# Performance work log

Measured on AMD Instinct MI355X. Metric: run time of the kernel, lower is better.

The kernel has to match this reference:

```python
import jax, jax.numpy as jnp
import numpy as np
from jax import lax

# ---- static config (matches init_kwargs) ----
ORDER = 1
NPTS = ORDER + 1            # 2
JUNC_K = 300
LINE_K = 5000
NMS_SIZE = 3
JUNC_THRESH = 0.008
EPS = 1e-5
B, C, H, W = 4, 256, 160, 160
HID = C // 4                # 64
OUT_CH = [1, 1, 2, 1, 2, 4]  # lmap,jmap,joff,cmap,coff,lvec
NHEADS = len(OUT_CH)
MAXO = max(OUT_CH)          # pad conv2 out-channels to 4 per head
# channel-select indices from padded (NHEADS*MAXO) grouped-conv output
SEL = np.array([h * MAXO + c for h, k in enumerate(OUT_CH) for c in range(k)])
# lvec channel permutation from original forward (identity for order=1)
PERM = np.arange(OUT_CH[-1]).reshape(-1, 2, 2)
PERM[:, 1] = PERM[::-1, 1]
PERM = PERM.reshape(-1)


def setup_inputs() -> dict:
    key = jax.random.key(0)
    ks = jax.random.split(key, 9)
    features = jax.random.normal(ks[0], (B, C, H, W), jnp.float32)
    w1 = jax.random.normal(ks[1], (NHEADS * HID, C, 3, 3), jnp.float32) / np.sqrt(C * 9)
    b1 = 0.01 * jax.random.normal(ks[2], (NHEADS * HID,), jnp.float32)
    gamma = 1.0 + 0.1 * jax.random.normal(ks[3], (NHEADS * HID,), jnp.float32)
    beta = 0.01 * jax.random.normal(ks[4], (NHEADS * HID,), jnp.float32)
    mean = 0.1 * jax.random.normal(ks[5], (NHEADS * HID,), jnp.float32)
    var = jax.random.uniform(ks[6], (NHEADS * HID,), jnp.float32, 0.5, 1.5)
    w2 = jax.random.normal(ks[7], (NHEADS * MAXO, HID, 3, 3), jnp.float32) / np.sqrt(HID * 9)
    b2 = 0.01 * jax.random.normal(ks[8], (NHEADS * MAXO,), jnp.float32)
    return dict(features=features, w1=w1, b1=b1, gamma=gamma, beta=beta,
                mean=mean, var=var, w2=w2, b2=b2)


def _conv(x, w, b, groups=1):
    y = lax.conv_general_dilated(x, w, (1, 1), 'SAME',
                                 dimension_numbers=('NCHW', 'OIHW', 'NCHW'),
                                 feature_group_count=groups)
    return y + b[None, :, None, None]


def _nms(hm):  # hm: (1,H,W) -> suppress non-peaks
    mx = lax.reduce_window(hm, -jnp.inf, lax.max, (1, NMS_SIZE, NMS_SIZE),
                           (1, 1, 1), [(0, 0), (1, 1), (1, 1)])
    return jnp.where(hm == mx, hm, 0.0)


def _post(jm, joff, cm, coff, lv):
    """Per-sample postprocess. jm,cm:(1,H,W) joff,coff:(2,H,W) lv:(4,H,W).
    Returns (pts:(LINE_K,2,2) padded lines, mask:(LINE_K,) validity)."""
    # junctions: NMS + top-K + thresh mask + offset gather
    sj, ij = lax.top_k(_nms(jm).reshape(-1), JUNC_K)
    valid_j = sj >= JUNC_THRESH
    xy = jnp.stack([ij % W, ij // W], -1).astype(jm.dtype)
    junc = xy + joff.reshape(2, -1).T[ij] + 0.5
    junc = jnp.stack([jnp.clip(junc[:, 0], 0.0, W - 1e-4),
                      jnp.clip(junc[:, 1], 0.0, H - 1e-4)], -1)
    # lines: top-K centers + vector field gather (thresh=0 -> always full K)
    sc, ic = lax.top_k(cm.reshape(-1), LINE_K)
    cxy = jnp.stack([ic % W, ic // W], -1).astype(cm.dtype)
    center = cxy + coff.reshape(2, -1).T[ic] + 0.5
    lvr = lv.reshape(NPTS // 2 * 2, 2, -1).transpose(2, 0, 1)  # (HW,2,2)
    loi = center[:, None] + lvr[ic]                            # (L,2,2)
    loi = jnp.stack([jnp.clip(loi[..., 0], 0.0, W - 1e-4),
                     jnp.clip(loi[..., 1], 0.0, H - 1e-4)], -1)
    # pairwise squared-distance argmin of each endpoint to junctions
    d1 = ((loi[:, None, 0] - junc[None]) ** 2).sum(-1)
    d2 = ((loi[:, None, -1] - junc[None]) ** 2).sum(-1)
    big = jnp.asarray(1e18, d1.dtype)
    i1 = jnp.argmin(jnp.where(valid_j[None], d1, big), axis=-1)
    i2 = jnp.argmin(jnp.where(valid_j[None], d2, big), axis=-1)
    imin = jnp.minimum(i1, i2)
    imax = jnp.maximum(i1, i2)
    keep = imin != imax
    # unique (imin,imax) pairs via sorted-key dedup (matches torch.unique order)
    BIGK = JUNC_K * JUNC_K
    keyv = jnp.where(keep, imin * JUNC_K + imax, BIGK)
    sk = jnp.sort(keyv)
    first = jnp.concatenate([jnp.ones((1,), bool), sk[1:] != sk[:-1]]) & (sk < BIGK)
    a = jnp.where(first, sk // JUNC_K, 0)
    b = jnp.where(first, sk % JUNC_K, 0)
    pts = jnp.stack([junc[a], junc[b]], axis=1)  # (L,2,2)
    swap = pts[:, 0, 1] > pts[:, 1, 1]
    pts = jnp.where(swap[:, None, None], pts[:, ::-1], pts)
    return pts, first


def _maps(features, w1, b1, gamma, beta, mean, var, w2, b2):
    y = _conv(features, w1, b1)
    y = (y - mean[None, :, None, None]) * gamma[None, :, None, None] * \
        lax.rsqrt(var + EPS)[None, :, None, None] + beta[None, :, None, None]
    y = jax.nn.relu(y)
    y = _conv(y, w2, b2, groups=NHEADS)        # (B, NHEADS*MAXO, H, W)
    m = y[:, SEL]                              # (B, 11, H, W)
    lmap = jax.nn.sigmoid(m[:, 0:1])
    jmap = jax.nn.sigmoid(m[:, 1:2])
    joff = m[:, 2:4]
    cmap = jax.nn.sigmoid(m[:, 4:5])
    coff = m[:, 5:7]
    lvec = m[:, 7:][:, PERM]
    return lmap, jmap, joff, cmap, coff, lvec


def reference(features, w1, b1, gamma, beta, mean, var, w2, b2):
    lmap, jmap, joff, cmap, coff, lvec = _maps(features, w1, b1, gamma, beta,
                                               mean, var, w2, b2)
    loi, mask = jax.vmap(_post)(jmap, joff, cmap, coff, lvec)
    return lmap, jmap, joff, cmap, coff, lvec, loi, mask


if __name__ == '__main__':
    out = reference(**setup_inputs())
    for o in out:
        print(o.shape, o.dtype)
```

## Files before the change

### kernel.cpp

```cpp
#include <hip/hip_runtime.h>
#include <math.h>

#define IMG   160
#define HWSZ  25600
#define NB    4
#define CIN   256
#define COUT1 384
#define BIGK  90000

#define OFF_LMAP 0
#define OFF_JMAP 102400
#define OFF_JOFF 204800
#define OFF_CMAP 409600
#define OFF_COFF 512000
#define OFF_LVEC 716800
#define OFF_LOI  1126400
#define OFF_MASK 1206400

static const size_t WS_Y1    = 0;
static const size_t WS_JSORT = (size_t)NB * COUT1 * HWSZ * 4;
static const size_t WS_CSORT = WS_JSORT + (size_t)NB * 32768 * 8;
static const size_t WS_JUNC  = WS_CSORT + (size_t)NB * 32768 * 8;
static const size_t WS_JVAL  = WS_JUNC + (size_t)NB * 300 * 2 * 4;
static const size_t WS_LKEY  = WS_JVAL + (size_t)NB * 300 * 4;
static const size_t WS_WPK   = WS_LKEY + (size_t)NB * 8192 * 4;
static const size_t WS_AFTER_WPK = WS_WPK + (size_t)12 * 8 * 9 * 32 * 64 * 2;
static const size_t WS_BNS   = WS_AFTER_WPK;
static const size_t WS_JM    = WS_BNS + 384 * 4;
static const size_t WS_CM    = WS_JM + (size_t)NB * 300 * 8;
static const size_t WS_FPK   = WS_CM + (size_t)NB * 5000 * 8;
static const size_t WS_NEED_MIN = WS_FPK;
static const size_t WS_NEED_PK = WS_FPK + (size_t)NB * 8 * 162 * 162 * 128;

typedef unsigned long long u64;
typedef __attribute__((ext_vector_type(8))) short short8;
typedef __attribute__((ext_vector_type(4))) float f32x4;
typedef __attribute__((ext_vector_type(4))) int int4v;

union frag_u { short8 s8; u64 u[2]; int4v v; };

__device__ __forceinline__ float clip_coord(float v) {
    return fminf(fmaxf(v, 0.0f), 159.9999f);
}
__device__ __forceinline__ float sigmoidf(float v) {
    return 1.0f / (1.0f + expf(-v));
}
__device__ __forceinline__ unsigned short f2bf(float f) {
    unsigned u = __float_as_uint(f);
    return (unsigned short)((u + 0x7FFFu + ((u >> 16) & 1u)) >> 16);
}
__device__ __forceinline__ float bf2f(unsigned short h) {
    return __uint_as_float((unsigned)h << 16);
}

__device__ __forceinline__ void async_copy16(void* lds, const void* g) {
    __builtin_amdgcn_global_load_lds(
        (const __attribute__((address_space(1))) unsigned int*)g,
        (__attribute__((address_space(3))) unsigned int*)lds, 16, 0, 0);
}


__global__ void wpack_pk_kernel(const float* __restrict__ w1, short* __restrict__ wpk,
                                const float* __restrict__ gamma,
                                const float* __restrict__ var,
                                float* __restrict__ bns) {
    if (blockIdx.x == 6912) {
        for (int i = threadIdx.x; i < COUT1; i += 256)
            bns[i] = gamma[i] / sqrtf(var[i] + 1e-5f);
        return;
    }
    int e = blockIdx.x * 256 + threadIdx.x;
    int row = e >> 6, sp = e & 63;
    int ocl = row & 31;
    int tap = (row >> 5) % 9;
    int icc = (row / 288) & 7;
    int octile = row / 2304;
    int p16 = sp >> 3, j = sp & 7;
    int l16 = p16 ^ (ocl & 7);
    int ql = l16 * 8 + j;
    int term = ql >> 5, icl = ql & 31;
    int oc = octile * 32 + ocl, ic = icc * 32 + icl;
    float a = w1[((size_t)oc * CIN + ic) * 9 + tap];
    unsigned short hi = f2bf(a);
    wpk[e] = (term == 0) ? (short)hi : (short)f2bf(a - bf2f(hi));
}

__global__ __launch_bounds__(256) void pack_feat_kernel(
    const float* __restrict__ feat, short* __restrict__ fpk) {
    const int tid = threadIdx.x;
    const int c4  = (tid >> 4) & 3;
    const int r0  = (tid & 15) | (((tid >> 6) & 3) << 4);
    const int rest = blockIdx.x * 64 + r0;
    const int px = rest % 162;
    const int t2 = rest / 162;
    const int py = t2 % 162;
    const int bi = t2 / 162;
    const int s  = (2 * py + px) & 7;
    const int gy = py - 1, gx = px - 1;
    const bool valid = ((unsigned)gy < (unsigned)IMG) && ((unsigned)gx < (unsigned)IMG);
    const float* fs = feat + (size_t)(bi * 32 + c4 * 8) * HWSZ
                           + (valid ? gy * IMG + gx : 0);
    unsigned hi4[4], lo4[4];
#pragma unroll
    for (int j2 = 0; j2 < 4; ++j2) {
        float va = valid ? fs[(size_t)(2 * j2) * HWSZ]     : 0.0f;
        float vb = valid ? fs[(size_t)(2 * j2 + 1) * HWSZ] : 0.0f;
        unsigned short ha = f2bf(va), hb = f2bf(vb);
        unsigned short la = f2bf(va - bf2f(ha)), lb = f2bf(vb - bf2f(hb));
        hi4[j2] = (unsigned)ha | ((unsigned)hb << 16);
        lo4[j2] = (unsigned)la | ((unsigned)lb << 16);
    }
    const int p0 = c4 ^ s;
    const int p1 = (c4 | 4) ^ s;
    int4v* base = (int4v*)(fpk + (size_t)rest * 64);
    base[p0] = (int4v){ (int)hi4[0], (int)hi4[1], (int)hi4[2], (int)hi4[3] };
    base[p1] = (int4v){ (int)lo4[0], (int)lo4[1], (int)lo4[2], (int)lo4[3] };
}

__global__ __launch_bounds__(256, 2) void conv1_mfma_pk(
    const short* __restrict__ fpk, const short* __restrict__ wpk,
    const float* __restrict__ b1, const float* __restrict__ bns,
    const float* __restrict__ beta, const float* __restrict__ mean,
    float* __restrict__ y1) {
    const int bid   = blockIdx.x;
    const int slot  = bid >> 3;
    const int tile  = (bid & 7) + ((slot / 12) << 3);
    const int octile = slot - (slot / 12) * 12;
    const int bb = tile / 100, tt = tile % 100;
    const int ty = (tt / 10) * 16, tx = (tt % 10) * 16;
    const int oc0 = octile * 32;
    const int tid  = threadIdx.x;
    const int w    = tid >> 6;
    const int lane = tid & 63;
    const int quad = lane >> 4;
    const int l15  = lane & 15;
    const int wbase = tid & 192;

    __shared__ __align__(16) short Alds[288 * 64];
    __shared__ __align__(16) short Blds[324 * 64];

    int aoff[2];
#pragma unroll
    for (int t = 0; t < 2; ++t)
        aoff[t] = l15 * 128 + ((((t << 2) | quad) ^ (l15 & 7)) << 4);

    f32x4 acc[2][4];
#pragma unroll
    for (int mi = 0; mi < 2; ++mi)
#pragma unroll
        for (int nj = 0; nj < 4; ++nj) acc[mi][nj] = (f32x4){0.f, 0.f, 0.f, 0.f};

    const char* asrc0 = (const char*)wpk + (size_t)(octile * 8) * 36864;

    int boff[10];
#pragma unroll
    for (int it = 0; it < 10; ++it) {
        int k = it * 256 + tid;
        int hy = (int)((unsigned)k / 144u);
        int r  = k - hy * 144;
        boff[it] = hy * (162 * 128) + r * 16;
    }
    const int roff = 17 * (162 * 128) + (112 + (tid & 31)) * 16;
    const char* bsrc0 = (const char*)fpk
        + (((size_t)(bb * 8) * 162 + ty) * 162 + tx) * 128;
    const size_t bstride = (size_t)162 * 162 * 128;

    {
#pragma unroll
        for (int i = 0; i < 9; ++i)
            async_copy16((char*)Alds + (size_t)(i * 256 + wbase) * 16,
                         asrc0 + (size_t)(i * 256 + tid) * 16);
#pragma unroll
        for (int it = 0; it < 10; ++it)
            async_copy16((char*)Blds + (size_t)(it * 256 + wbase) * 16,
                         bsrc0 + boff[it]);
        if (tid < 32) {
            const int4v vv = *(const int4v*)(bsrc0 + roff);
            *(int4v*)((char*)Blds + (size_t)(2560 + tid) * 16) = vv;
        }
    }
    __syncthreads();

    int4v pvB[10]; int4v pvR;
#pragma unroll 1
    for (int icc = 0; icc < 8; ++icc) {
        if (icc < 7) {
            const char* bs = bsrc0 + (size_t)(icc + 1) * bstride;
#pragma unroll
            for (int it = 0; it < 10; ++it)
                pvB[it] = *(const int4v*)(bs + boff[it]);
            pvR = *(const int4v*)(bs + roff);
        }

#pragma unroll
        for (int sx = 0; sx < 3; ++sx) {
            frag_u Bf[2][6];
#pragma unroll
            for (int t = 0; t < 2; ++t)
#pragma unroll
                for (int rr = 0; rr < 6; ++rr) {
                    int pos = (w * 4 + rr) * 18 + (l15 + sx);
                    const char* bp = (const char*)Blds + (size_t)pos * 128
                        + ((((t << 2) | quad) ^ (pos & 7)) << 4);
                    Bf[t][rr].v = *(const int4v*)bp;
                }
#pragma unroll
            for (int sy = 0; sy < 3; ++sy) {
                const int tap = sy * 3 + sx;
                frag_u Af[2][2];
#pragma unroll
                for (int t = 0; t < 2; ++t)
#pragma unroll
                    for (int mi = 0; mi < 2; ++mi) {
                        const char* ap = (const char*)Alds
                            + (size_t)(tap * 32 + mi * 16) * 128 + aoff[t];
                        Af[t][mi].v = *(const int4v*)ap;
                    }
#pragma unroll
                for (int mi = 0; mi < 2; ++mi)
#pragma unroll
                    for (int nj = 0; nj < 4; ++nj) {
                        acc[mi][nj] = __builtin_amdgcn_mfma_f32_16x16x32_bf16(
                            Af[0][mi].s8, Bf[0][nj + sy].s8, acc[mi][nj], 0, 0, 0);
                        acc[mi][nj] = __builtin_amdgcn_mfma_f32_16x16x32_bf16(
                            Af[0][mi].s8, Bf[1][nj + sy].s8, acc[mi][nj], 0, 0, 0);
                        acc[mi][nj] = __builtin_amdgcn_mfma_f32_16x16x32_bf16(
                            Af[1][mi].s8, Bf[0][nj + sy].s8, acc[mi][nj], 0, 0, 0);
                    }
            }
        }

        if (icc < 7) {
            __syncthreads();
            {
                const char* as = asrc0 + (size_t)(icc + 1) * 36864;
#pragma unroll
                for (int i = 0; i < 9; ++i)
                    async_copy16((char*)Alds + (size_t)(i * 256 + wbase) * 16,
                                 as + (size_t)(i * 256 + tid) * 16);
            }
#pragma unroll
            for (int it = 0; it < 10; ++it)
                *(int4v*)((char*)Blds + (size_t)(it * 256 + tid) * 16) = pvB[it];
            if (tid < 32)
                *(int4v*)((char*)Blds + (size_t)(2560 + tid) * 16) = pvR;
            __syncthreads();
        }
    }

#pragma unroll
    for (int nj = 0; nj < 4; ++nj) {
        const int gy = ty + w * 4 + nj, gx = tx + l15;
#pragma unroll
        for (int mi = 0; mi < 2; ++mi)
#pragma unroll
            for (int r = 0; r < 4; ++r) {
                const int oc = oc0 + mi * 16 + quad * 4 + r;
                float v = acc[mi][nj][r] + b1[oc];
                v = (v - mean[oc]) * bns[oc] + beta[oc];
                y1[((size_t)(bb * COUT1 + oc)) * HWSZ + gy * IMG + gx] = fmaxf(v, 0.0f);
            }
    }
}


__global__ void wpack_kernel(const float* __restrict__ w1, short* __restrict__ wpk) {
    int e = blockIdx.x * 256 + threadIdx.x;
    int row = e >> 6, sp = e & 63;
    int ocl = row & 31;
    int tap = (row >> 5) % 9;
    int icc = (row / 288) & 7;
    int octile = row / 2304;
    int s = (sp >> 2) ^ (ocl & 15);
    int ql = s * 4 + (sp & 3);
    int term = ql >> 5, icl = ql & 31;
    int oc = octile * 32 + ocl, ic = icc * 32 + icl;
    float a = w1[((size_t)oc * CIN + ic) * 9 + tap];
    unsigned short hi = f2bf(a);
    wpk[e] = (term == 0) ? (short)hi : (short)f2bf(a - bf2f(hi));
}

__global__ __launch_bounds__(256, 2) void conv1_mfma(
    const float* __restrict__ feat, const short* __restrict__ wpk,
    const float* __restrict__ b1, const float* __restrict__ gamma,
    const float* __restrict__ beta, const float* __restrict__ mean,
    const float* __restrict__ var, float* __restrict__ y1) {
    const int bid   = blockIdx.x;
    const int slot  = bid >> 3;
    const int tile  = (bid & 7) + ((slot / 12) << 3);
    const int octile = slot - (slot / 12) * 12;
    const int bb = tile / 100, tt = tile % 100;
    const int ty = (tt / 10) * 16, tx = (tt % 10) * 16;
    const int oc0 = octile * 32;
    const int tid  = threadIdx.x;
    const int w    = tid >> 6;
    const int lane = tid & 63;
    const int quad = lane >> 4;
    const int l15  = lane & 15;

    __shared__ short Alds[288 * 64];
    __shared__ short Blds[324 * 68];

    int aoff[2][2];
#pragma unroll
    for (int t = 0; t < 2; ++t)
#pragma unroll
        for (int h = 0; h < 2; ++h)
            aoff[t][h] = l15 * 128 + (((t * 8 + quad * 2 + h) ^ l15) * 8);

    f32x4 acc[2][4];
#pragma unroll
    for (int mi = 0; mi < 2; ++mi)
#pragma unroll
        for (int nj = 0; nj < 4; ++nj) acc[mi][nj] = (f32x4){0.f, 0.f, 0.f, 0.f};

    const int4v* asrc_base = (const int4v*)wpk + (size_t)(octile * 8) * 2304;
    unsigned* Bd = (unsigned*)Blds;

    float pv0[21], pv1[21];

#pragma unroll
    for (int ii = 0; ii < 21; ++ii) {
        int i = tid + ii * 256;
        if (i < 5184) {
            int icp = i / 324, hp = i - icp * 324;
            int hy = hp / 18, hx = hp - hy * 18;
            int gy = ty + hy - 1, gx = tx + hx - 1;
            bool valid = ((unsigned)gy < IMG) && ((unsigned)gx < IMG);
            const float* fs = feat + ((size_t)(bb * CIN + icp * 2)) * HWSZ
                                   + (valid ? (gy * IMG + gx) : 0);
            pv0[ii] = valid ? fs[0]    : 0.0f;
            pv1[ii] = valid ? fs[HWSZ] : 0.0f;
        }
    }

#pragma unroll 1
    for (int icc = 0; icc < 8; ++icc) {
        __syncthreads();
        {
            const int4v* asrc = asrc_base + (size_t)icc * 2304;
            int4v* adst = (int4v*)Alds;
#pragma unroll
            for (int i = 0; i < 9; ++i)
                adst[tid + i * 256] = asrc[tid + i * 256];
        }
#pragma unroll
        for (int ii = 0; ii < 21; ++ii) {
            int i = tid + ii * 256;
            if (i < 5184) {
                int icp = i / 324, hp = i - icp * 324;
                float v0 = pv0[ii], v1 = pv1[ii];
                unsigned short h0 = f2bf(v0), h1 = f2bf(v1);
                unsigned short m0 = f2bf(v0 - bf2f(h0)), m1 = f2bf(v1 - bf2f(h1));
                Bd[hp * 34 + icp]      = (unsigned)h0 | ((unsigned)h1 << 16);
                Bd[hp * 34 + 16 + icp] = (unsigned)m0 | ((unsigned)m1 << 16);
            }
        }
        __syncthreads();

        if (icc < 7) {
#pragma unroll
            for (int ii = 0; ii < 21; ++ii) {
                int i = tid + ii * 256;
                if (i < 5184) {
                    int icp = i / 324, hp = i - icp * 324;
                    int hy = hp / 18, hx = hp - hy * 18;
                    int gy = ty + hy - 1, gx = tx + hx - 1;
                    bool valid = ((unsigned)gy < IMG) && ((unsigned)gx < IMG);
                    const float* fs = feat
                        + ((size_t)(bb * CIN + (icc + 1) * 32 + icp * 2)) * HWSZ
                        + (valid ? (gy * IMG + gx) : 0);
                    pv0[ii] = valid ? fs[0]    : 0.0f;
                    pv1[ii] = valid ? fs[HWSZ] : 0.0f;
                }
            }
        }

#pragma unroll
        for (int tap = 0; tap < 9; ++tap) {
            const int sy = tap / 3, sx = tap % 3;
            frag_u Af[2][2], Bf[2][4];
#pragma unroll
            for (int t = 0; t < 2; ++t) {
#pragma unroll
                for (int mi = 0; mi < 2; ++mi) {
                    const char* base = (const char*)Alds + (tap * 32 + mi * 16) * 128;
                    Af[t][mi].u[0] = *(const u64*)(base + aoff[t][0]);
                    Af[t][mi].u[1] = *(const u64*)(base + aoff[t][1]);
                }
#pragma unroll
                for (int nj = 0; nj < 4; ++nj) {
                    int pos = (w * 4 + nj + sy) * 18 + (l15 + sx);
                    const short* bp = &Blds[pos * 68 + t * 32 + quad * 8];
                    Bf[t][nj].u[0] = *(const u64*)bp;
                    Bf[t][nj].u[1] = *(const u64*)(bp + 4);
                }
            }
#pragma unroll
            for (int mi = 0; mi < 2; ++mi)
#pragma unroll
                for (int nj = 0; nj < 4; ++nj) {
                    acc[mi][nj] = __builtin_amdgcn_mfma_f32_16x16x32_bf16(
                        Af[0][mi].s8, Bf[0][nj].s8, acc[mi][nj], 0, 0, 0);
                    acc[mi][nj] = __builtin_amdgcn_mfma_f32_16x16x32_bf16(
                        Af[0][mi].s8, Bf[1][nj].s8, acc[mi][nj], 0, 0, 0);
                    acc[mi][nj] = __builtin_amdgcn_mfma_f32_16x16x32_bf16(
                        Af[1][mi].s8, Bf[0][nj].s8, acc[mi][nj], 0, 0, 0);
                    acc[mi][nj] = __builtin_amdgcn_mfma_f32_16x16x32_bf16(
                        Af[1][mi].s8, Bf[1][nj].s8, acc[mi][nj], 0, 0, 0);
                }
        }
    }

#pragma unroll
    for (int nj = 0; nj < 4; ++nj) {
        const int gy = ty + w * 4 + nj, gx = tx + l15;
#pragma unroll
        for (int mi = 0; mi < 2; ++mi)
#pragma unroll
            for (int r = 0; r < 4; ++r) {
                const int oc = oc0 + mi * 16 + quad * 4 + r;
                float v = acc[mi][nj][r] + b1[oc];
                v = (v - mean[oc]) * (gamma[oc] / sqrtf(var[oc] + 1e-5f)) + beta[oc];
                y1[((size_t)(bb * COUT1 + oc)) * HWSZ + gy * IMG + gx] = fmaxf(v, 0.0f);
            }
    }
}


__global__ __launch_bounds__(256, 2) void conv2_kernel(
    const float* __restrict__ y1, const float* __restrict__ w2,
    const float* __restrict__ b2, float* __restrict__ out) {
    const int KH[6]   = {1, 1, 2, 1, 2, 4};
    const int REG[6]  = {OFF_LMAP, OFF_JMAP, OFF_JOFF, OFF_CMAP, OFF_COFF, OFF_LVEC};
    const int SIGF[6] = {1, 1, 0, 1, 0, 0};

    const int bz = blockIdx.z;
    const int b  = bz / 6;
    const int h  = bz % 6;
    const int k  = KH[h];
    const int tx = blockIdx.x * 32, ty = blockIdx.y * 16;
    const int lx = threadIdx.x, ly = threadIdx.y;
    const int tid = ly * 16 + lx;

    __shared__ float tin[16][18][40];
    float* const tinf = &tin[0][0][0];
    float accv[4][2] = {{0.f,0.f},{0.f,0.f},{0.f,0.f},{0.f,0.f}};

    const float* yb = y1 + ((size_t)(b * COUT1 + h * 64)) * HWSZ;

    bool sok[3], sval[3];
    int  soff[3], sidx[3];
#pragma unroll
    for (int j = 0; j < 3; ++j) {
        int idx = tid + j * 256;
        sok[j] = (idx < 612);
        int r = idx / 34, col = idx - r * 34;
        int gy = ty - 1 + r, gx = tx - 1 + col;
        sval[j] = sok[j] && ((unsigned)gy < (unsigned)IMG) && ((unsigned)gx < (unsigned)IMG);
        soff[j] = sval[j] ? (gy * IMG + gx) : 0;
        sidx[j] = r * 40 + col;
    }

    for (int ic0 = 0; ic0 < 64; ic0 += 16) {
        __syncthreads();
#pragma unroll
        for (int j = 0; j < 3; ++j) {
            if (sok[j]) {
                const float* yp = yb + (size_t)ic0 * HWSZ + soff[j];
                float* tp = tinf + sidx[j];
#pragma unroll 4
                for (int c = 0; c < 16; ++c)
                    tp[c * 720] = sval[j] ? yp[(size_t)c * HWSZ] : 0.0f;
            }
        }
        __syncthreads();

        const float* tb = tinf + ly * 40 + 2 * lx;
#pragma unroll 2
        for (int c = 0; c < 16; ++c) {
            const float* tc = tb + c * 720;
            float n[3][4];
#pragma unroll
            for (int r = 0; r < 3; ++r) {
                float2 u = *(const float2*)(tc + r * 40);
                float2 v = *(const float2*)(tc + r * 40 + 2);
                n[r][0] = u.x; n[r][1] = u.y; n[r][2] = v.x; n[r][3] = v.y;
            }
#pragma unroll
            for (int o = 0; o < 4; ++o) {
                if (o < k) {
                    const float* wp = w2 + ((size_t)((h * 4 + o) * 64 + (ic0 + c))) * 9;
                    float a0 = accv[o][0], a1 = accv[o][1];
#pragma unroll
                    for (int r = 0; r < 3; ++r) {
                        float w0 = wp[3*r], w1 = wp[3*r+1], w2v = wp[3*r+2];
                        a0 = fmaf(n[r][0], w0, a0);
                        a1 = fmaf(n[r][1], w0, a1);
                        a0 = fmaf(n[r][1], w1, a0);
                        a1 = fmaf(n[r][2], w1, a1);
                        a0 = fmaf(n[r][2], w2v, a0);
                        a1 = fmaf(n[r][3], w2v, a1);
                    }
                    accv[o][0] = a0; accv[o][1] = a1;
                }
            }
        }
    }

    const int p = (ty + ly) * IMG + tx + 2 * lx;
#pragma unroll
    for (int o = 0; o < 4; ++o) {
        if (o < k) {
            float v0 = accv[o][0] + b2[h * 4 + o];
            float v1 = accv[o][1] + b2[h * 4 + o];
            if (SIGF[h]) { v0 = sigmoidf(v0); v1 = sigmoidf(v1); }
            size_t base = (size_t)REG[h] + ((size_t)(b * k + o)) * HWSZ + p;
            out[base]     = v0;
            out[base + 1] = v1;
        }
    }
}

__global__ void nms_pack_kernel(const float* __restrict__ out,
                                u64* __restrict__ jsort,
                                u64* __restrict__ csort) {
    const int g = blockIdx.x;
    const int b = g / 100, q = g % 100;
    const int p = q * 256 + threadIdx.x;
    const float* jm = out + OFF_JMAP + (size_t)b * HWSZ;
    const float* cm = out + OFF_CMAP + (size_t)b * HWSZ;

    const int x = p % IMG, y = p / IMG;
    float v = jm[p];
    float mx = v;
#pragma unroll
    for (int dy = -1; dy <= 1; ++dy)
#pragma unroll
        for (int dx = -1; dx <= 1; ++dx) {
            int nx = x + dx, ny = y + dy;
            if (nx >= 0 && nx < IMG && ny >= 0 && ny < IMG)
                mx = fmaxf(mx, jm[ny * IMG + nx]);
        }
    float nmsv = (v == mx) ? v : 0.0f;

    u64 tagj = ((u64)__float_as_uint(nmsv) << 32)
             | (u64)(0xFFFFFFFFu - (unsigned)p);
    u64 tagc = ((u64)__float_as_uint(cm[p]) << 32)
             | (u64)(0xFFFFFFFFu - (unsigned)p);
    jsort[(size_t)b * 32768 + p] = tagj;
    csort[(size_t)b * 32768 + p] = tagc;
    if (q < 28) {
        int pp = 25600 + q * 256 + threadIdx.x;
        jsort[(size_t)b * 32768 + pp] = 0ull;
        csort[(size_t)b * 32768 + pp] = 0ull;
    }
}

#define SK64(i) ((i) + ((i) >> 4))
__global__ __launch_bounds__(1024) void sort64_ldsA(u64* __restrict__ buf) {
    __shared__ u64 s[8192 + 512];
    const size_t base = (size_t)blockIdx.x * 8192;
    for (int i = threadIdx.x; i < 8192; i += 1024) s[SK64(i)] = buf[base + i];
    for (int k = 2; k <= 8192; k <<= 1)
        for (int j = k >> 1; j > 0; j >>= 1) {
            __syncthreads();
            for (int t = threadIdx.x; t < 4096; t += 1024) {
                int i = ((t & ~(j - 1)) << 1) | (t & (j - 1));
                int l = i | j;
                bool desc = ((i & k) == 0);
                u64 x = s[SK64(i)], y = s[SK64(l)];
                if (desc ? (x < y) : (x > y)) { s[SK64(i)] = y; s[SK64(l)] = x; }
            }
        }
    __syncthreads();
    for (int i = threadIdx.x; i < 8192; i += 1024) buf[base + i] = s[SK64(i)];
}

__device__ __forceinline__ int count_gt_desc(const u64* __restrict__ a, u64 e) {
    int cnt = 0;
#pragma unroll
    for (int st = 8192; st > 0; st >>= 1)
        if (cnt + st <= 8192 && a[cnt + st - 1] > e) cnt += st;
    return cnt;
}

__global__ void merge_topk_kernel(const u64* __restrict__ jsort,
                                  const u64* __restrict__ csort,
                                  u64* __restrict__ jm, u64* __restrict__ cm) {
    const int b = blockIdx.y;
    int t = blockIdx.x * 256 + threadIdx.x;
    const u64* src; u64* dst; int K, chunk, pos;
    if (t < 1200) {
        src = jsort + (size_t)b * 32768; dst = jm + (size_t)b * 300;
        K = 300; chunk = t / 300; pos = t - chunk * 300;
    } else {
        t -= 1200;
        if (t >= 20000) return;
        src = csort + (size_t)b * 32768; dst = cm + (size_t)b * 5000;
        K = 5000; chunk = t / 5000; pos = t - chunk * 5000;
    }
    u64 e = src[chunk * 8192 + pos];
    int rank = pos;
#pragma unroll
    for (int c = 0; c < 4; ++c)
        if (c != chunk) rank += count_gt_desc(src + c * 8192, e);
    if (rank < K) dst[rank] = e;
}

__global__ __launch_bounds__(1024) void sort32_lds(int* __restrict__ buf) {
    __shared__ int s[8192];
    int* a = buf + (size_t)blockIdx.x * 8192;
    for (int i = threadIdx.x; i < 8192; i += 1024) s[i] = a[i];
    for (int k = 2; k <= 8192; k <<= 1)
        for (int j = k >> 1; j > 0; j >>= 1) {
            __syncthreads();
            for (int t = threadIdx.x; t < 4096; t += 1024) {
                int i = ((t & ~(j - 1)) << 1) | (t & (j - 1));
                int l = i | j;
                bool asc = ((i & k) == 0);
                int x = s[i], y = s[l];
                if (asc ? (x > y) : (x < y)) { s[i] = y; s[l] = x; }
            }
        }
    __syncthreads();
    for (int i = threadIdx.x; i < 8192; i += 1024) a[i] = s[i];
}

__global__ void junction_kernel(const u64* __restrict__ jmk,
                                const float* __restrict__ out,
                                float* __restrict__ junc, int* __restrict__ jvalid) {
    const int b = blockIdx.x;
    const int t = threadIdx.x;
    if (t >= 300) return;
    u64 key = jmk[(size_t)b * 300 + t];
    float score  = __uint_as_float((unsigned)(key >> 32));
    unsigned idx = 0xFFFFFFFFu - (unsigned)(key & 0xFFFFFFFFull);
    const float* j0 = out + OFF_JOFF + (size_t)(b * 2) * HWSZ;
    const float* j1 = j0 + HWSZ;
    float jx = (float)(idx % IMG) + j0[idx] + 0.5f;
    float jy = (float)(idx / IMG) + j1[idx] + 0.5f;
    junc[(size_t)(b * 300 + t) * 2]     = clip_coord(jx);
    junc[(size_t)(b * 300 + t) * 2 + 1] = clip_coord(jy);
    jvalid[b * 300 + t] = (score >= 0.008f) ? 1 : 0;
}

__global__ void lines_kernel(const u64* __restrict__ cmk,
                             const float* __restrict__ junc,
                             const int* __restrict__ jvalid,
                             const float* __restrict__ out,
                             int* __restrict__ lkeys) {
    const int b = blockIdx.y;
    const int t = blockIdx.x * 256 + threadIdx.x;

    __shared__ float jx[300], jy[300];
    __shared__ int jv[300];
    for (int i = threadIdx.x; i < 300; i += 256) {
        jx[i] = junc[(size_t)(b * 300 + i) * 2];
        jy[i] = junc[(size_t)(b * 300 + i) * 2 + 1];
        jv[i] = jvalid[b * 300 + i];
    }
    __syncthreads();

    if (t >= 8192) return;
    if (t >= 5000) { lkeys[b * 8192 + t] = 0x7FFFFFFF; return; }

    u64 key = cmk[(size_t)b * 5000 + t];
    unsigned idx = 0xFFFFFFFFu - (unsigned)(key & 0xFFFFFFFFull);
    const float* c0 = out + OFF_COFF + (size_t)(b * 2) * HWSZ;
    const float* c1 = c0 + HWSZ;
    const float* lv = out + OFF_LVEC + (size_t)(b * 4) * HWSZ;

    float cx = (float)(idx % IMG) + c0[idx] + 0.5f;
    float cy = (float)(idx / IMG) + c1[idx] + 0.5f;
    float e0x = clip_coord(cx + lv[idx]);
    float e0y = clip_coord(cy + lv[HWSZ + idx]);
    float e1x = clip_coord(cx + lv[2 * HWSZ + idx]);
    float e1y = clip_coord(cy + lv[3 * HWSZ + idx]);

    float m1 = 1e18f, m2 = 1e18f;
    int i1 = 0, i2 = 0;
    for (int j = 0; j < 300; ++j) {
        if (jv[j]) {
            float dx = e0x - jx[j], dy = e0y - jy[j];
            float d = dx * dx + dy * dy;
            if (d < m1) { m1 = d; i1 = j; }
            dx = e1x - jx[j]; dy = e1y - jy[j];
            d = dx * dx + dy * dy;
            if (d < m2) { m2 = d; i2 = j; }
        }
    }
    int imin = min(i1, i2), imax = max(i1, i2);
    lkeys[b * 8192 + t] = (i1 != i2) ? (imin * 300 + imax) : BIGK;
}

__global__ void finalize_kernel(const int* __restrict__ lkeys,
                                const float* __restrict__ junc,
                                float* __restrict__ out) {
    const int b = blockIdx.y;
    const int t = blockIdx.x * 256 + threadIdx.x;
    if (t >= 5000) return;
    const int* lk = lkeys + b * 8192;
    int sk = lk[t];
    bool first = ((t == 0) || (sk != lk[t - 1])) && (sk < BIGK);
    int a  = first ? sk / 300 : 0;
    int bb = first ? sk % 300 : 0;
    float p0x = junc[(size_t)(b * 300 + a) * 2];
    float p0y = junc[(size_t)(b * 300 + a) * 2 + 1];
    float p1x = junc[(size_t)(b * 300 + bb) * 2];
    float p1y = junc[(size_t)(b * 300 + bb) * 2 + 1];
    if (p0y > p1y) {
        float tx = p0x; p0x = p1x; p1x = tx;
        float ty = p0y; p0y = p1y; p1y = ty;
    }
    size_t base = OFF_LOI + (size_t)(b * 5000 + t) * 4;
    out[base]     = p0x;
    out[base + 1] = p0y;
    out[base + 2] = p1x;
    out[base + 3] = p1y;
    out[OFF_MASK + b * 5000 + t] = first ? 1.0f : 0.0f;
}

extern "C" void kernel_launch(void* const* d_in, const int* in_sizes, int n_in,
                              void* d_out, int out_size, void* d_ws, size_t ws_size,
                              hipStream_t stream) {
    const float* feat  = (const float*)d_in[0];
    const float* w1    = (const float*)d_in[1];
    const float* b1    = (const float*)d_in[2];
    const float* gamma = (const float*)d_in[3];
    const float* beta  = (const float*)d_in[4];
    const float* mean  = (const float*)d_in[5];
    const float* var   = (const float*)d_in[6];
    const float* w2    = (const float*)d_in[7];
    const float* b2    = (const float*)d_in[8];
    float* out = (float*)d_out;
    char*  ws  = (char*)d_ws;

    if (ws_size < WS_NEED_MIN) return;

    float* y1 = (float*)(ws + WS_Y1);
    u64* jsort = (u64*)(ws + WS_JSORT);
    float* junc = (float*)(ws + WS_JUNC);
    int* jvalid = (int*)(ws + WS_JVAL);
    int* lkeys  = (int*)(ws + WS_LKEY);
    u64* csort = (u64*)(ws + WS_CSORT);
    short* wpk = (short*)(ws + WS_WPK);
    float* bns = (float*)(ws + WS_BNS);
    u64* jm    = (u64*)(ws + WS_JM);
    u64* cm    = (u64*)(ws + WS_CM);
    short* fpk = (short*)(ws + WS_FPK);

    if (ws_size >= WS_NEED_PK) {
        wpack_pk_kernel<<<dim3(6913), dim3(256), 0, stream>>>(w1, wpk, gamma, var, bns);
        pack_feat_kernel<<<dim3(13122), dim3(256), 0, stream>>>(feat, fpk);
        conv1_mfma_pk<<<dim3(4800), dim3(256), 0, stream>>>(
            fpk, wpk, b1, bns, beta, mean, y1);
    } else {
        wpack_kernel<<<dim3(6912), dim3(256), 0, stream>>>(w1, wpk);
        conv1_mfma<<<dim3(4800), dim3(256), 0, stream>>>(
            feat, wpk, b1, gamma, beta, mean, var, y1);
    }

    conv2_kernel<<<dim3(5, 10, NB * 6), dim3(16, 16), 0, stream>>>(y1, w2, b2, out);

    nms_pack_kernel<<<dim3(NB * 100), dim3(256), 0, stream>>>(out, jsort, csort);

    sort64_ldsA<<<dim3(32), dim3(1024), 0, stream>>>(jsort);

    merge_topk_kernel<<<dim3(83, NB), dim3(256), 0, stream>>>(jsort, csort, jm, cm);

    junction_kernel<<<dim3(NB), dim3(320), 0, stream>>>(jm, out, junc, jvalid);

    lines_kernel<<<dim3(32, NB), dim3(256), 0, stream>>>(cm, junc, jvalid, out, lkeys);

    sort32_lds<<<dim3(NB), dim3(1024), 0, stream>>>(lkeys);

    finalize_kernel<<<dim3(20, NB), dim3(256), 0, stream>>>(lkeys, junc, out);
}
```

Measured before the change: 950.4 us.

## Fuse prep, NMS+sort, and junction kernels; widen conv1 tiles with double-buffered weights

Merges weight packing, BN-scale and feature packing into one prep launch. It also folds the NMS key packing into the bitonic sort kernel, and removes the junction kernel by recomputing junction coordinates inside the lines and finalize kernels. conv1 now uses 512-thread blocks covering 16x32 output tiles, which shares the halo between two column halves. It double-buffers the weight tile in LDS so the next weight chunk streams in during compute. This cuts launch count and redundant global traffic, in exchange for higher LDS use per block and repeated coordinate recomputation in finalize.

Result: slower. 1.006 ms (+5.8%).

```diff
diff --git a/kernel.cpp b/kernel.cpp
--- a/kernel.cpp
+++ b/kernel.cpp
@@ -60,37 +60,38 @@
 }
 
 
-__global__ void wpack_pk_kernel(const float* __restrict__ w1, short* __restrict__ wpk,
-                                const float* __restrict__ gamma,
-                                const float* __restrict__ var,
-                                float* __restrict__ bns) {
-    if (blockIdx.x == 6912) {
-        for (int i = threadIdx.x; i < COUT1; i += 256)
+__global__ __launch_bounds__(256) void prep_kernel(
+    const float* __restrict__ w1, short* __restrict__ wpk,
+    const float* __restrict__ gamma, const float* __restrict__ var,
+    float* __restrict__ bns,
+    const float* __restrict__ feat, short* __restrict__ fpk) {
+    const int blk = blockIdx.x;
+    const int tid = threadIdx.x;
+    if (blk < 6912) {
+        int e = blk * 256 + tid;
+        int row = e >> 6, sp = e & 63;
+        int ocl = row & 31;
+        int tap = (row >> 5) % 9;
+        int icc = (row / 288) & 7;
+        int octile = row / 2304;
+        int p16 = sp >> 3, j = sp & 7;
+        int l16 = p16 ^ (ocl & 7);
+        int ql = l16 * 8 + j;
+        int term = ql >> 5, icl = ql & 31;
+        int oc = octile * 32 + ocl, ic = icc * 32 + icl;
+        float a = w1[((size_t)oc * CIN + ic) * 9 + tap];
+        unsigned short hi = f2bf(a);
+        wpk[e] = (term == 0) ? (short)hi : (short)f2bf(a - bf2f(hi));
+        return;
+    }
+    if (blk == 6912) {
+        for (int i = tid; i < COUT1; i += 256)
             bns[i] = gamma[i] / sqrtf(var[i] + 1e-5f);
         return;
     }
-    int e = blockIdx.x * 256 + threadIdx.x;
-    int row = e >> 6, sp = e & 63;
-    int ocl = row & 31;
-    int tap = (row >> 5) % 9;
-    int icc = (row / 288) & 7;
-    int octile = row / 2304;
-    int p16 = sp >> 3, j = sp & 7;
-    int l16 = p16 ^ (ocl & 7);
-    int ql = l16 * 8 + j;
-    int term = ql >> 5, icl = ql & 31;
-    int oc = octile * 32 + ocl, ic = icc * 32 + icl;
-    float a = w1[((size_t)oc * CIN + ic) * 9 + tap];
-    unsigned short hi = f2bf(a);
-    wpk[e] = (term == 0) ? (short)hi : (short)f2bf(a - bf2f(hi));
-}
-
-__global__ __launch_bounds__(256) void pack_feat_kernel(
-    const float* __restrict__ feat, short* __restrict__ fpk) {
-    const int tid = threadIdx.x;
     const int c4  = (tid >> 4) & 3;
     const int r0  = (tid & 15) | (((tid >> 6) & 3) << 4);
-    const int rest = blockIdx.x * 64 + r0;
+    const int rest = (blk - 6913) * 64 + r0;
     const int px = rest % 162;
     const int t2 = rest / 162;
     const int py = t2 % 162;
@@ -117,7 +118,7 @@
     base[p1] = (int4v){ (int)lo4[0], (int)lo4[1], (int)lo4[2], (int)lo4[3] };
 }
 
-__global__ __launch_bounds__(256, 2) void conv1_mfma_pk(
+__global__ __launch_bounds__(512, 2) void conv1_mfma_pk(
     const short* __restrict__ fpk, const short* __restrict__ wpk,
     const float* __restrict__ b1, const float* __restrict__ bns,
     const float* __restrict__ beta, const float* __restrict__ mean,
@@ -126,18 +127,20 @@
     const int slot  = bid >> 3;
     const int tile  = (bid & 7) + ((slot / 12) << 3);
     const int octile = slot - (slot / 12) * 12;
-    const int bb = tile / 100, tt = tile % 100;
-    const int ty = (tt / 10) * 16, tx = (tt % 10) * 16;
+    const int bb = tile / 50, tt = tile % 50;
+    const int ty = (tt / 5) * 16, tx = (tt % 5) * 32;
     const int oc0 = octile * 32;
     const int tid  = threadIdx.x;
-    const int w    = tid >> 6;
+    const int wid  = tid >> 6;
+    const int wr   = wid >> 1;
+    const int wc   = wid & 1;
     const int lane = tid & 63;
     const int quad = lane >> 4;
     const int l15  = lane & 15;
-    const int wbase = tid & 192;
-
-    __shared__ __align__(16) short Alds[288 * 64];
-    __shared__ __align__(16) short Blds[324 * 64];
+    const int wbase = tid & ~63;
+
+    __shared__ __align__(16) short Alds[2][288 * 64];
+    __shared__ __align__(16) short Blds[612 * 64];
 
     int aoff[2];
 #pragma unroll
@@ -155,41 +158,56 @@
     int boff[10];
 #pragma unroll
     for (int it = 0; it < 10; ++it) {
-        int k = it * 256 + tid;
-        int hy = (int)((unsigned)k / 144u);
-        int r  = k - hy * 144;
+        int k = it * 512 + tid;
+        int hy = (int)((unsigned)k / 272u);
+        int r  = k - hy * 272;
         boff[it] = hy * (162 * 128) + r * 16;
     }
-    const int roff = 17 * (162 * 128) + (112 + (tid & 31)) * 16;
     const char* bsrc0 = (const char*)fpk
         + (((size_t)(bb * 8) * 162 + ty) * 162 + tx) * 128;
     const size_t bstride = (size_t)162 * 162 * 128;
 
     {
-#pragma unroll
-        for (int i = 0; i < 9; ++i)
-            async_copy16((char*)Alds + (size_t)(i * 256 + wbase) * 16,
-                         asrc0 + (size_t)(i * 256 + tid) * 16);
-#pragma unroll
-        for (int it = 0; it < 10; ++it)
-            async_copy16((char*)Blds + (size_t)(it * 256 + wbase) * 16,
+        char* ad = (char*)&Alds[0][0];
+#pragma unroll
+        for (int i = 0; i < 4; ++i)
+            async_copy16(ad + (size_t)(i * 512 + wbase) * 16,
+                         asrc0 + (size_t)(i * 512 + tid) * 16);
+        if (tid < 256)
+            async_copy16(ad + (size_t)(2048 + wbase) * 16,
+                         asrc0 + (size_t)(2048 + tid) * 16);
+#pragma unroll
+        for (int it = 0; it < 9; ++it)
+            async_copy16((char*)Blds + (size_t)(it * 512 + wbase) * 16,
                          bsrc0 + boff[it]);
-        if (tid < 32) {
-            const int4v vv = *(const int4v*)(bsrc0 + roff);
-            *(int4v*)((char*)Blds + (size_t)(2560 + tid) * 16) = vv;
+        if (tid < 288) {
+            const int4v vv = *(const int4v*)(bsrc0 + boff[9]);
+            *(int4v*)((char*)Blds + (size_t)(4608 + tid) * 16) = vv;
         }
     }
     __syncthreads();
 
-    int4v pvB[10]; int4v pvR;
+    int4v pvB[10];
 #pragma unroll 1
     for (int icc = 0; icc < 8; ++icc) {
+        const int cur = icc & 1;
+        const char* Ab = (const char*)&Alds[cur][0];
+
         if (icc < 7) {
+            const char* as = asrc0 + (size_t)(icc + 1) * 36864;
+            char* ad = (char*)&Alds[cur ^ 1][0];
+#pragma unroll
+            for (int i = 0; i < 4; ++i)
+                async_copy16(ad + (size_t)(i * 512 + wbase) * 16,
+                             as + (size_t)(i * 512 + tid) * 16);
+            if (tid < 256)
+                async_copy16(ad + (size_t)(2048 + wbase) * 16,
+                             as + (size_t)(2048 + tid) * 16);
             const char* bs = bsrc0 + (size_t)(icc + 1) * bstride;
 #pragma unroll
-            for (int it = 0; it < 10; ++it)
+            for (int it = 0; it < 9; ++it)
                 pvB[it] = *(const int4v*)(bs + boff[it]);
-            pvR = *(const int4v*)(bs + roff);
+            if (tid < 288) pvB[9] = *(const int4v*)(bs + boff[9]);
         }
 
 #pragma unroll
@@ -199,7 +217,7 @@
             for (int t = 0; t < 2; ++t)
 #pragma unroll
                 for (int rr = 0; rr < 6; ++rr) {
-                    int pos = (w * 4 + rr) * 18 + (l15 + sx);
+                    int pos = (wr * 4 + rr) * 34 + (wc * 16 + l15 + sx);
                     const char* bp = (const char*)Blds + (size_t)pos * 128
                         + ((((t << 2) | quad) ^ (pos & 7)) << 4);
                     Bf[t][rr].v = *(const int4v*)bp;
@@ -212,7 +230,7 @@
                 for (int t = 0; t < 2; ++t)
 #pragma unroll
                     for (int mi = 0; mi < 2; ++mi) {
-                        const char* ap = (const char*)Alds
+                        const char* ap = Ab
                             + (size_t)(tap * 32 + mi * 16) * 128 + aoff[t];
                         Af[t][mi].v = *(const int4v*)ap;
                     }
@@ -232,25 +250,18 @@
 
         if (icc < 7) {
             __syncthreads();
-            {
-                const char* as = asrc0 + (size_t)(icc + 1) * 36864;
-#pragma unroll
-                for (int i = 0; i < 9; ++i)
-                    async_copy16((char*)Alds + (size_t)(i * 256 + wbase) * 16,
-                                 as + (size_t)(i * 256 + tid) * 16);
-            }
-#pragma unroll
-            for (int it = 0; it < 10; ++it)
-                *(int4v*)((char*)Blds + (size_t)(it * 256 + tid) * 16) = pvB[it];
-            if (tid < 32)
-                *(int4v*)((char*)Blds + (size_t)(2560 + tid) * 16) = pvR;
+#pragma unroll
+            for (int it = 0; it < 9; ++it)
+                *(int4v*)((char*)Blds + (size_t)(it * 512 + tid) * 16) = pvB[it];
+            if (tid < 288)
+                *(int4v*)((char*)Blds + (size_t)(4608 + tid) * 16) = pvB[9];
             __syncthreads();
         }
     }
 
 #pragma unroll
     for (int nj = 0; nj < 4; ++nj) {
-        const int gy = ty + w * 4 + nj, gx = tx + l15;
+        const int gy = ty + wr * 4 + nj, gx = tx + wc * 16 + l15;
 #pragma unroll
         for (int mi = 0; mi < 2; ++mi)
 #pragma unroll
@@ -522,46 +533,40 @@
     }
 }
 
-__global__ void nms_pack_kernel(const float* __restrict__ out,
-                                u64* __restrict__ jsort,
-                                u64* __restrict__ csort) {
-    const int g = blockIdx.x;
-    const int b = g / 100, q = g % 100;
-    const int p = q * 256 + threadIdx.x;
-    const float* jm = out + OFF_JMAP + (size_t)b * HWSZ;
-    const float* cm = out + OFF_CMAP + (size_t)b * HWSZ;
-
-    const int x = p % IMG, y = p / IMG;
-    float v = jm[p];
-    float mx = v;
-#pragma unroll
-    for (int dy = -1; dy <= 1; ++dy)
-#pragma unroll
-        for (int dx = -1; dx <= 1; ++dx) {
-            int nx = x + dx, ny = y + dy;
-            if (nx >= 0 && nx < IMG && ny >= 0 && ny < IMG)
-                mx = fmaxf(mx, jm[ny * IMG + nx]);
-        }
-    float nmsv = (v == mx) ? v : 0.0f;
-
-    u64 tagj = ((u64)__float_as_uint(nmsv) << 32)
-             | (u64)(0xFFFFFFFFu - (unsigned)p);
-    u64 tagc = ((u64)__float_as_uint(cm[p]) << 32)
-             | (u64)(0xFFFFFFFFu - (unsigned)p);
-    jsort[(size_t)b * 32768 + p] = tagj;
-    csort[(size_t)b * 32768 + p] = tagc;
-    if (q < 28) {
-        int pp = 25600 + q * 256 + threadIdx.x;
-        jsort[(size_t)b * 32768 + pp] = 0ull;
-        csort[(size_t)b * 32768 + pp] = 0ull;
-    }
-}
-
 #define SK64(i) ((i) + ((i) >> 4))
-__global__ __launch_bounds__(1024) void sort64_ldsA(u64* __restrict__ buf) {
+__global__ __launch_bounds__(1024) void sortnms_kernel(
+    const float* __restrict__ out, u64* __restrict__ buf) {
     __shared__ u64 s[8192 + 512];
-    const size_t base = (size_t)blockIdx.x * 8192;
-    for (int i = threadIdx.x; i < 8192; i += 1024) s[SK64(i)] = buf[base + i];
+    const int bid = blockIdx.x;
+    const int arr = bid >> 2, chunk = bid & 3;
+    const bool isj = (arr < 4);
+    const int b = arr & 3;
+    const float* mp = out + (isj ? OFF_JMAP : OFF_CMAP) + (size_t)b * HWSZ;
+
+    for (int i = threadIdx.x; i < 8192; i += 1024) {
+        int p = chunk * 8192 + i;
+        u64 key = 0ull;
+        if (p < HWSZ) {
+            float v = mp[p];
+            float nv = v;
+            if (isj) {
+                const int x = p % IMG, y = p / IMG;
+                float mx = v;
+#pragma unroll
+                for (int dy = -1; dy <= 1; ++dy)
+#pragma unroll
+                    for (int dx = -1; dx <= 1; ++dx) {
+                        int nx = x + dx, ny = y + dy;
+                        if (nx >= 0 && nx < IMG && ny >= 0 && ny < IMG)
+                            mx = fmaxf(mx, mp[ny * IMG + nx]);
+                    }
+                nv = (v == mx) ? v : 0.0f;
+            }
+            key = ((u64)__float_as_uint(nv) << 32)
+                | (u64)(0xFFFFFFFFu - (unsigned)p);
+        }
+        s[SK64(i)] = key;
+    }
     for (int k = 2; k <= 8192; k <<= 1)
         for (int j = k >> 1; j > 0; j >>= 1) {
             __syncthreads();
@@ -574,6 +579,7 @@
             }
         }
     __syncthreads();
+    const size_t base = (size_t)bid * 8192;
     for (int i = threadIdx.x; i < 8192; i += 1024) buf[base + i] = s[SK64(i)];
 }
 
@@ -627,27 +633,8 @@
     for (int i = threadIdx.x; i < 8192; i += 1024) a[i] = s[i];
 }
 
-__global__ void junction_kernel(const u64* __restrict__ jmk,
-                                const float* __restrict__ out,
-                                float* __restrict__ junc, int* __restrict__ jvalid) {
-    const int b = blockIdx.x;
-    const int t = threadIdx.x;
-    if (t >= 300) return;
-    u64 key = jmk[(size_t)b * 300 + t];
-    float score  = __uint_as_float((unsigned)(key >> 32));
-    unsigned idx = 0xFFFFFFFFu - (unsigned)(key & 0xFFFFFFFFull);
-    const float* j0 = out + OFF_JOFF + (size_t)(b * 2) * HWSZ;
-    const float* j1 = j0 + HWSZ;
-    float jx = (float)(idx % IMG) + j0[idx] + 0.5f;
-    float jy = (float)(idx / IMG) + j1[idx] + 0.5f;
-    junc[(size_t)(b * 300 + t) * 2]     = clip_coord(jx);
-    junc[(size_t)(b * 300 + t) * 2 + 1] = clip_coord(jy);
-    jvalid[b * 300 + t] = (score >= 0.008f) ? 1 : 0;
-}
-
 __global__ void lines_kernel(const u64* __restrict__ cmk,
-                             const float* __restrict__ junc,
-                             const int* __restrict__ jvalid,
+                             const u64* __restrict__ jmk,
                              const float* __restrict__ out,
                              int* __restrict__ lkeys) {
     const int b = blockIdx.y;
@@ -655,10 +642,17 @@
 
     __shared__ float jx[300], jy[300];
     __shared__ int jv[300];
-    for (int i = threadIdx.x; i < 300; i += 256) {
-        jx[i] = junc[(size_t)(b * 300 + i) * 2];
-        jy[i] = junc[(size_t)(b * 300 + i) * 2 + 1];
-        jv[i] = jvalid[b * 300 + i];
+    {
+        const float* j0 = out + OFF_JOFF + (size_t)(b * 2) * HWSZ;
+        const float* j1 = j0 + HWSZ;
+        for (int i = threadIdx.x; i < 300; i += 256) {
+            u64 key = jmk[(size_t)b * 300 + i];
+            float score  = __uint_as_float((unsigned)(key >> 32));
+            unsigned idx = 0xFFFFFFFFu - (unsigned)(key & 0xFFFFFFFFull);
+            jx[i] = clip_coord((float)(idx % IMG) + j0[idx] + 0.5f);
+            jy[i] = clip_coord((float)(idx / IMG) + j1[idx] + 0.5f);
+            jv[i] = (score >= 0.008f) ? 1 : 0;
+        }
     }
     __syncthreads();
 
@@ -695,7 +689,7 @@
 }
 
 __global__ void finalize_kernel(const int* __restrict__ lkeys,
-                                const float* __restrict__ junc,
+                                const u64* __restrict__ jmk,
                                 float* __restrict__ out) {
     const int b = blockIdx.y;
     const int t = blockIdx.x * 256 + threadIdx.x;
@@ -705,10 +699,16 @@
     bool first = ((t == 0) || (sk != lk[t - 1])) && (sk < BIGK);
     int a  = first ? sk / 300 : 0;
     int bb = first ? sk % 300 : 0;
-    float p0x = junc[(size_t)(b * 300 + a) * 2];
-    float p0y = junc[(size_t)(b * 300 + a) * 2 + 1];
-    float p1x = junc[(size_t)(b * 300 + bb) * 2];
-    float p1y = junc[(size_t)(b * 300 + bb) * 2 + 1];
+    const float* j0 = out + OFF_JOFF + (size_t)(b * 2) * HWSZ;
+    const float* j1 = j0 + HWSZ;
+    u64 ka = jmk[(size_t)b * 300 + a];
+    u64 kb = jmk[(size_t)b * 300 + bb];
+    unsigned ia = 0xFFFFFFFFu - (unsigned)(ka & 0xFFFFFFFFull);
+    unsigned ib = 0xFFFFFFFFu - (unsigned)(kb & 0xFFFFFFFFull);
+    float p0x = clip_coord((float)(ia % IMG) + j0[ia] + 0.5f);
+    float p0y = clip_coord((float)(ia / IMG) + j1[ia] + 0.5f);
+    float p1x = clip_coord((float)(ib % IMG) + j0[ib] + 0.5f);
+    float p1y = clip_coord((float)(ib / IMG) + j1[ib] + 0.5f);
     if (p0y > p1y) {
         float tx = p0x; p0x = p1x; p1x = tx;
         float ty = p0y; p0y = p1y; p1y = ty;
@@ -740,8 +740,6 @@
 
     float* y1 = (float*)(ws + WS_Y1);
     u64* jsort = (u64*)(ws + WS_JSORT);
-    float* junc = (float*)(ws + WS_JUNC);
-    int* jvalid = (int*)(ws + WS_JVAL);
     int* lkeys  = (int*)(ws + WS_LKEY);
     u64* csort = (u64*)(ws + WS_CSORT);
     short* wpk = (short*)(ws + WS_WPK);
@@ -751,9 +749,9 @@
     short* fpk = (short*)(ws + WS_FPK);
 
     if (ws_size >= WS_NEED_PK) {
-        wpack_pk_kernel<<<dim3(6913), dim3(256), 0, stream>>>(w1, wpk, gamma, var, bns);
-        pack_feat_kernel<<<dim3(13122), dim3(256), 0, stream>>>(feat, fpk);
-        conv1_mfma_pk<<<dim3(4800), dim3(256), 0, stream>>>(
+        prep_kernel<<<dim3(20035), dim3(256), 0, stream>>>(
+            w1, wpk, gamma, var, bns, feat, fpk);
+        conv1_mfma_pk<<<dim3(2400), dim3(512), 0, stream>>>(
             fpk, wpk, b1, bns, beta, mean, y1);
     } else {
         wpack_kernel<<<dim3(6912), dim3(256), 0, stream>>>(w1, wpk);
@@ -763,17 +761,13 @@
 
     conv2_kernel<<<dim3(5, 10, NB * 6), dim3(16, 16), 0, stream>>>(y1, w2, b2, out);
 
-    nms_pack_kernel<<<dim3(NB * 100), dim3(256), 0, stream>>>(out, jsort, csort);
-
-    sort64_ldsA<<<dim3(32), dim3(1024), 0, stream>>>(jsort);
+    sortnms_kernel<<<dim3(32), dim3(1024), 0, stream>>>(out, jsort);
 
     merge_topk_kernel<<<dim3(83, NB), dim3(256), 0, stream>>>(jsort, csort, jm, cm);
 
-    junction_kernel<<<dim3(NB), dim3(320), 0, stream>>>(jm, out, junc, jvalid);
-
-    lines_kernel<<<dim3(32, NB), dim3(256), 0, stream>>>(cm, junc, jvalid, out, lkeys);
+    lines_kernel<<<dim3(32, NB), dim3(256), 0, stream>>>(cm, jm, out, lkeys);
 
     sort32_lds<<<dim3(NB), dim3(1024), 0, stream>>>(lkeys);
 
-    finalize_kernel<<<dim3(20, NB), dim3(256), 0, stream>>>(lkeys, junc, out);
-}
+    finalize_kernel<<<dim3(20, NB), dim3(256), 0, stream>>>(lkeys, jm, out);
+}
```
